# Performance work log

Hardware: AMD Instinct MI355X
Metric: run time of the kernel (lower is better)

Reference implementation:

```python
import jax, jax.numpy as jnp
import numpy as np

POOL = 7  # adaptive_avg_pool2d output size (7,7)


def _bin_edges(start, length):
    """Adaptive-avg-pool bin boundaries.
    start, length: [N] int32 -> (lo, hi) each [N, POOL] absolute indices,
    matching torch: lo_i = floor(i*L/P), hi_i = ceil((i+1)*L/P).
    """
    i = jnp.arange(POOL, dtype=jnp.int32)
    lo = start[:, None] + (i[None, :] * length[:, None]) // POOL
    hi = start[:, None] + (-((-(i[None, :] + 1)) * length[:, None] // POOL))
    # note: ceil(a/b) = -(-a // b); written below explicitly
    hi = start[:, None] - ((-(i[None, :] + 1) * length[:, None]) // POOL)
    return lo, hi


def roi_adaptive_avg_pool(features, rois):
    """features: [1, C, H, W]; rois: [N, 4] int (x1,y1,x2,y2 inclusive).
    Returns [N, C, POOL, POOL] == torch stack of adaptive_avg_pool2d over
    features[:, :, y1:y2+1, x1:x2+1], vectorized via an integral image.
    """
    B, C, H, W = features.shape  # B == 1 (forced by shared_fcs input dim)
    # integral image with a zero row/col prepended: ii[y, x] = sum over [:y, :x]
    ii = jnp.cumsum(jnp.cumsum(features, axis=2), axis=3)
    ii = jnp.pad(ii, ((0, 0), (0, 0), (1, 0), (1, 0)))[0]  # [C, H+1, W+1]

    x1, y1, x2, y2 = rois[:, 0], rois[:, 1], rois[:, 2], rois[:, 3]
    ys, ye = _bin_edges(y1, y2 - y1 + 1)   # [N, POOL]
    xs, xe = _bin_edges(x1, x2 - x1 + 1)
    Y0, Y1 = ys[:, :, None], ye[:, :, None]   # [N, POOL, 1]
    X0, X1 = xs[:, None, :], xe[:, None, :]   # [N, 1, POOL]

    def gather(Y, X):
        return ii[:, Y, X]  # [C, N, POOL, POOL]

    sums = gather(Y1, X1) - gather(Y0, X1) - gather(Y1, X0) + gather(Y0, X0)
    area = ((Y1 - Y0) * (X1 - X0)).astype(features.dtype)  # [N, POOL, POOL]
    pooled = sums / area[None]                              # [C, N, POOL, POOL]
    return jnp.transpose(pooled, (1, 0, 2, 3))              # [N, C, POOL, POOL]


def setup_inputs() -> dict:
    key = jax.random.key(0)
    ks = jax.random.split(key, 12)
    C, H, W, N, F = 256, 336, 336, 2000, 256
    features = jax.random.normal(ks[0], (1, C, H, W), dtype=jnp.float32)
    # valid small ROIs (shuttlecock-sized), x1<=x2, y1<=y2, in-bounds
    x1 = jax.random.randint(ks[1], (N,), 0, W - 40)
    y1 = jax.random.randint(ks[2], (N,), 0, H - 40)
    bw = jax.random.randint(ks[3], (N,), 4, 40)
    bh = jax.random.randint(ks[4], (N,), 4, 40)
    rois = jnp.stack([x1, y1, jnp.minimum(x1 + bw, W - 1),
                      jnp.minimum(y1 + bh, H - 1)], axis=1).astype(jnp.int32)
    d_in = C * POOL * POOL
    w1 = jax.random.normal(ks[5], (d_in, F), dtype=jnp.float32) * (1.0 / np.sqrt(d_in))
    b1 = jnp.zeros((F,), dtype=jnp.float32)
    w2 = jax.random.normal(ks[6], (F, F), dtype=jnp.float32) * (1.0 / np.sqrt(F))
    b2 = jnp.zeros((F,), dtype=jnp.float32)
    w_cls = jax.random.normal(ks[7], (F, 2), dtype=jnp.float32) * 0.01
    b_cls = jnp.zeros((2,), dtype=jnp.float32)
    w_reg = jax.random.normal(ks[8], (F, 4), dtype=jnp.float32) * 0.001
    b_reg = jnp.zeros((4,), dtype=jnp.float32)
    return {"features": features, "rois": rois, "w1": w1, "b1": b1,
            "w2": w2, "b2": b2, "w_cls": w_cls, "b_cls": b_cls,
            "w_reg": w_reg, "b_reg": b_reg}


def reference(features, rois, w1, b1, w2, b2, w_cls, b_cls, w_reg, b_reg):
    roi_feats = roi_adaptive_avg_pool(features, rois)          # [N, C, 7, 7]
    roi_feats = roi_feats.reshape(roi_feats.shape[0], -1)      # [N, C*49]
    h = jax.nn.relu(roi_feats @ w1 + b1)
    h = jax.nn.relu(h @ w2 + b2)
    cls_score = h @ w_cls + b_cls                              # [N, num_classes+1]
    bbox_pred = h @ w_reg + b_reg                              # [N, 4]
    return (cls_score, bbox_pred)
```

## Files before the change

kernel.cpp:

```cpp
#include <hip/hip_runtime.h>

typedef unsigned int uint;
typedef unsigned short ushort;
typedef __bf16 v8bf __attribute__((ext_vector_type(8)));
typedef float v4f __attribute__((ext_vector_type(4)));
typedef float f2 __attribute__((ext_vector_type(2)));
typedef float f4v __attribute__((ext_vector_type(4)));

#define CCH 256
#define HH 336
#define WW 336
#define HWSZ (HH*WW)
#define NROI 2000
#define KDIM 12544
#define MPAD 2048
#define SPLITK 7
#define KSP (KDIM/SPLITK)
#define NTRB (HWSZ/64)

__device__ __forceinline__ ushort bf16r(float f) {
  uint u = __float_as_uint(f);
  u += 0x7fffu + ((u >> 16) & 1u);
  return (ushort)(u >> 16);
}
__device__ __forceinline__ uint packbf(float a, float b) {
  return (uint)bf16r(a) | ((uint)bf16r(b) << 16);
}

typedef const __attribute__((address_space(1))) uint* gas_t;
typedef __attribute__((address_space(3))) uint* las_t;
__device__ __forceinline__ void async16(const void* g, void* l) {
  __builtin_amdgcn_global_load_lds((gas_t)g, (las_t)l, 16, 0, 0);
}

#define GLOAD4(dst, ptr)                                             \
  asm volatile("global_load_dwordx4 %0, %1, off" : "=v"(dst) : "v"(ptr))

__global__ __launch_bounds__(256) void k_trprep(const float* __restrict__ f,
                                                uint* __restrict__ ftu,
                                                const float* __restrict__ w1,
                                                uint* __restrict__ w1t_u,
                                                const float* __restrict__ w2,
                                                ushort* __restrict__ w2t,
                                                const int* __restrict__ rois,
                                                int* __restrict__ perm) {
  __shared__ uint SM[64 * 128];
  int tid = threadIdx.x;
  if (blockIdx.x < NTRB) {
    uint* T = SM;
    int hw0 = blockIdx.x * 64;
    int hwq = tid & 15;
    int cp = tid >> 4;
    const float* base = f + hw0 + hwq * 4;
    f4v va[8], vb[8];
#pragma unroll
    for (int j = 0; j < 8; ++j) {
      int cpair = j * 16 + cp;
      const float* pa = base + (size_t)(2 * cpair) * HWSZ;
      GLOAD4(va[j], pa);
      GLOAD4(vb[j], pa + HWSZ);
    }
    asm volatile("s_waitcnt vmcnt(0)" ::: "memory");
    __builtin_amdgcn_sched_barrier(0);
    int sw = (hwq & 7) << 2;
#pragma unroll
    for (int j = 0; j < 8; ++j) {
      int cs = (j * 16 + cp) ^ sw;
      T[(hwq * 4 + 0) * 128 + cs] = packbf(va[j].x, vb[j].x);
      T[(hwq * 4 + 1) * 128 + cs] = packbf(va[j].y, vb[j].y);
      T[(hwq * 4 + 2) * 128 + cs] = packbf(va[j].z, vb[j].z);
      T[(hwq * 4 + 3) * 128 + cs] = packbf(va[j].w, vb[j].w);
    }
    __syncthreads();
    int co = tid & 31, r = tid >> 5;
#pragma unroll
    for (int i = 0; i < 8; ++i) {
      int row = i * 8 + r;
      int col = (co * 4) ^ (((row >> 2) & 7) << 2);
      uint4 v = *(const uint4*)&T[row * 128 + col];
      *(uint4*)(ftu + (size_t)(hw0 + row) * 128 + co * 4) = v;
    }
    return;
  }
  int b = blockIdx.x - NTRB;
  if (b < 392) {
    ushort (*T)[258] = reinterpret_cast<ushort (*)[258]>(SM);
    int bin = b % 49;
    int c0 = (b / 49) * 32;
    int n = tid;
    for (int i = 0; i < 32; ++i)
      T[i][n] = bf16r(w1[(size_t)((c0 + i) * 49 + bin) * 256 + n]);
    __syncthreads();
    int cc = tid & 15;
    int nb = tid >> 4;
    for (int rep = 0; rep < 16; ++rep) {
      int nn = rep * 16 + nb;
      uint v = (uint)T[2 * cc][nn] | ((uint)T[2 * cc + 1][nn] << 16);
      w1t_u[(size_t)nn * (KDIM / 2) + bin * 128 + c0 / 2 + cc] = v;
    }
  } else if (b < 424) {
    int n = (b - 392) * 8 + (tid >> 5);
    for (int kl = 0; kl < 8; ++kl) {
      int k = kl * 32 + (tid & 31);
      w2t[n * 256 + k] = bf16r(w2[k * 256 + n]);
    }
  } else {
    int* hist = (int*)((char*)SM + 16512);
    int* keys = hist + 64;
    if (tid < 64) hist[tid] = 0;
    __syncthreads();
    for (int i = tid; i < NROI; i += 256) {
      int x1 = rois[i * 4 + 0], y1 = rois[i * 4 + 1];
      int x2 = rois[i * 4 + 2], y2 = rois[i * 4 + 3];
      int cx = (x1 + x2) >> 1, cy = (y1 + y2) >> 1;
      int k = (cy / 42) * 8 + (cx / 42);
      keys[i] = k;
      atomicAdd(&hist[k], 1);
    }
    __syncthreads();
    if (tid < 64) {
      int v = hist[tid];
      int s = v;
#pragma unroll
      for (int d = 1; d < 64; d <<= 1) {
        int t2 = __shfl_up(s, d, 64);
        if (tid >= d) s += t2;
      }
      hist[tid] = s - v;
    }
    __syncthreads();
    for (int i = tid; i < NROI; i += 256) {
      int pos = atomicAdd(&hist[keys[i]], 1);
      perm[pos] = i;
    }
  }
}

__device__ __forceinline__ void pkacc(f2& acc, uint u) {
  f2 t;
  t.x = __uint_as_float(u << 16);
  t.y = __uint_as_float(u & 0xffff0000u);
  asm("v_pk_add_f32 %0, %1, %0" : "+v"(acc) : "v"(t));
}
#define UNPK2(S, u) do { pkacc(S[0], (u).x); pkacc(S[1], (u).y); } while (0)

#define GLOAD2(dst, ptr, OFF)                                        \
  asm volatile("global_load_dwordx2 %0, %1, off offset:" #OFF        \
               : "=v"(dst) : "v"(ptr))

template <int RH>
__device__ __forceinline__ void pool_unit(const uint2* __restrict__ ftu2,
                                          uint2* __restrict__ rfu2,
                                          int x1, int Lw, int ylo, int lane,
                                          uint ob) {
  const uint2* pr[RH];
#pragma unroll
  for (int r = 0; r < RH; ++r)
    pr[r] = ftu2 + (size_t)((ylo + r) * WW + x1) * 64 + lane;
  int xend = x1 + Lw;
  int b = 0;
  int lo_cur = x1;
  int hi_cur = x1 + (Lw + 6) / 7;
  int lo_next = x1 + Lw / 7;
  f2 P[2], Lc[2], Ln[2];
  P[0] = (f2){0.f, 0.f}; P[1] = (f2){0.f, 0.f};
  Lc[0] = (f2){0.f, 0.f}; Lc[1] = (f2){0.f, 0.f};
  Ln[0] = (f2){0.f, 0.f}; Ln[1] = (f2){0.f, 0.f};
  const float invr = 1.0f / (float)RH;
  for (int xc = x1; xc < xend; xc += 4) {
    uint2 v[4][RH];
#pragma unroll
    for (int r = 0; r < RH; ++r) {
      GLOAD2(v[0][r], pr[r], 0);
      GLOAD2(v[1][r], pr[r], 512);
      GLOAD2(v[2][r], pr[r], 1024);
      GLOAD2(v[3][r], pr[r], 1536);
    }
    asm volatile("s_waitcnt vmcnt(0)" ::: "memory");
    __builtin_amdgcn_sched_barrier(0);
#pragma unroll
    for (int r = 0; r < RH; ++r) pr[r] += 256;
#pragma unroll
    for (int c = 0; c < 4; ++c) {
      int x = xc + c;
      if (x < xend) {
#pragma unroll
        for (int r = 0; r < RH; ++r) UNPK2(P, v[c][r]);
        int xp = x + 1;
        if (xp == lo_next) { Ln[0] = P[0]; Ln[1] = P[1]; }
        while (b < 7 && xp == hi_cur) {
          float inv = invr / (float)(hi_cur - lo_cur);
          uint2 o;
          o.x = packbf((P[0].x - Lc[0].x) * inv, (P[0].y - Lc[0].y) * inv);
          o.y = packbf((P[1].x - Lc[1].x) * inv, (P[1].y - Lc[1].y) * inv);
          rfu2[ob + b * 64] = o;
          ++b;
          Lc[0] = Ln[0]; Lc[1] = Ln[1];
          lo_cur = lo_next;
          hi_cur = x1 + ((b + 1) * Lw + 6) / 7;
          lo_next = x1 + ((b + 1) * Lw) / 7;
          if (xp == lo_next) { Ln[0] = P[0]; Ln[1] = P[1]; }
        }
      }
    }
  }
}

__global__ __launch_bounds__(64) void k_pool(const int* __restrict__ rois,
                                             const int* __restrict__ perm,
                                             const uint2* __restrict__ ftu2,
                                             uint2* __restrict__ rfu2) {
  int L = blockIdx.x;
  int i = L >> 3;
  int slot = (L & 7) * 250 + i / 7;
  int by = i % 7;
  int n = perm[slot];
  int lane = threadIdx.x;
  int x1 = rois[n * 4 + 0], y1 = rois[n * 4 + 1];
  int x2 = rois[n * 4 + 2], y2 = rois[n * 4 + 3];
  int Lw = x2 - x1 + 1, Lh = y2 - y1 + 1;
  int ylo = y1 + (by * Lh) / 7;
  int yhi = y1 + ((by + 1) * Lh + 6) / 7;
  int rh = yhi - ylo;
  uint ob = ((uint)n * 49 + (uint)by * 7) * 64 + lane;
  switch (rh) {
    case 1: pool_unit<1>(ftu2, rfu2, x1, Lw, ylo, lane, ob); break;
    case 2: pool_unit<2>(ftu2, rfu2, x1, Lw, ylo, lane, ob); break;
    case 3: pool_unit<3>(ftu2, rfu2, x1, Lw, ylo, lane, ob); break;
    case 4: pool_unit<4>(ftu2, rfu2, x1, Lw, ylo, lane, ob); break;
    case 5: pool_unit<5>(ftu2, rfu2, x1, Lw, ylo, lane, ob); break;
    case 6: pool_unit<6>(ftu2, rfu2, x1, Lw, ylo, lane, ob); break;
    default: pool_unit<7>(ftu2, rfu2, x1, Lw, ylo, lane, ob); break;
  }
}

__global__ __launch_bounds__(256) void k_gemm1(const ushort* __restrict__ A,
                                               const ushort* __restrict__ B,
                                               float* __restrict__ P) {
  __shared__ ushort As[64 * 64];
  __shared__ ushort Bs[128 * 64];
  int m0 = blockIdx.x * 64;
  int n0 = blockIdx.y * 128;
  int ks = blockIdx.z;
  int k0 = ks * KSP;
  int tid = threadIdx.x;
  int lane = tid & 63, wv = tid >> 6;
  int wm = wv & 1, wn = wv >> 1;
  int lm = lane & 15, quad = lane >> 4;
  int srow = tid >> 3, scol = (tid & 7) * 8;
  v4f acc[2][4];
#pragma unroll
  for (int i = 0; i < 2; ++i)
#pragma unroll
    for (int j = 0; j < 4; ++j) acc[i][j] = (v4f){0.f, 0.f, 0.f, 0.f};
  const ushort* Ab = A + (size_t)(m0 + srow) * KDIM + k0 + scol;
  const ushort* Bb = B + (size_t)(n0 + srow) * KDIM + k0 + scol;
  for (int kt = 0; kt < KSP / 64; ++kt) {
    __syncthreads();
#pragma unroll
    for (int r = 0; r < 2; ++r)
      async16(Ab + (size_t)(r * 32) * KDIM + kt * 64, &As[(srow + r * 32) * 64 + scol]);
#pragma unroll
    for (int r = 0; r < 4; ++r)
      async16(Bb + (size_t)(r * 32) * KDIM + kt * 64, &Bs[(srow + r * 32) * 64 + scol]);
    __syncthreads();
#pragma unroll
    for (int kk = 0; kk < 64; kk += 32) {
      v8bf a[2], b[4];
#pragma unroll
      for (int i = 0; i < 2; ++i)
        a[i] = *(const v8bf*)&As[(wm * 32 + i * 16 + lm) * 64 + kk + quad * 8];
#pragma unroll
      for (int j = 0; j < 4; ++j)
        b[j] = *(const v8bf*)&Bs[(wn * 64 + j * 16 + lm) * 64 + kk + quad * 8];
#pragma unroll
      for (int i = 0; i < 2; ++i)
#pragma unroll
        for (int j = 0; j < 4; ++j)
          acc[i][j] = __builtin_amdgcn_mfma_f32_16x16x32_bf16(a[i], b[j], acc[i][j], 0, 0, 0);
    }
  }
  float* Pb = P + (size_t)ks * MPAD * 256;
#pragma unroll
  for (int i = 0; i < 2; ++i)
#pragma unroll
    for (int j = 0; j < 4; ++j) {
      int row = m0 + wm * 32 + i * 16 + quad * 4;
      int col = n0 + wn * 64 + j * 16 + lm;
#pragma unroll
      for (int r = 0; r < 4; ++r)
        Pb[(size_t)(row + r) * 256 + col] = acc[i][j][r];
    }
}

__global__ __launch_bounds__(256) void k_gemm2(const float* __restrict__ P,
                                               const float* __restrict__ b1,
                                               const ushort* __restrict__ w2t,
                                               const float* __restrict__ b2,
                                               const float* __restrict__ wcls,
                                               const float* __restrict__ bcls,
                                               const float* __restrict__ wreg,
                                               const float* __restrict__ breg,
                                               float* __restrict__ out) {
  __shared__ ushort HsA[64 * 256];
  __shared__ ushort Bs2[256 * 64];
  __shared__ float Hs[64 * 257];
  int tid = threadIdx.x;
  int r0 = blockIdx.x * 64;
  int lane = tid & 63, wv = tid >> 6;
  int lm = lane & 15, quad = lane >> 4;
  int srow = tid >> 3, scol = (tid & 7) * 8;
  uint* H = (uint*)HsA;
  for (int it = 0; it < 16; ++it) {
    int e = it * 256 + tid;
    int row = e >> 6;
    int c4 = e & 63;
    float4 s = {0.f, 0.f, 0.f, 0.f};
#pragma unroll
    for (int ks = 0; ks < SPLITK; ++ks) {
      float4 v = ((const float4*)P)[((size_t)ks * MPAD + r0 + row) * 64 + c4];
      s.x += v.x; s.y += v.y; s.z += v.z; s.w += v.w;
    }
    int col = c4 * 4;
    s.x = fmaxf(s.x + b1[col + 0], 0.f);
    s.y = fmaxf(s.y + b1[col + 1], 0.f);
    s.z = fmaxf(s.z + b1[col + 2], 0.f);
    s.w = fmaxf(s.w + b1[col + 3], 0.f);
    int cs = (c4 >> 1) ^ (row & 7);
    int ui = row * 128 + cs * 4 + (c4 & 1) * 2;
    H[ui]     = packbf(s.x, s.y);
    H[ui + 1] = packbf(s.z, s.w);
  }
  v4f acc[16];
#pragma unroll
  for (int j = 0; j < 16; ++j) acc[j] = (v4f){0.f, 0.f, 0.f, 0.f};
  int arow = wv * 16 + lm;
  int asw = (arow & 7) << 3;
  for (int kt = 0; kt < 4; ++kt) {
    __syncthreads();
#pragma unroll
    for (int r = 0; r < 8; ++r)
      async16(w2t + (size_t)(srow + r * 32) * 256 + kt * 64 + scol,
              &Bs2[(srow + r * 32) * 64 + scol]);
    __syncthreads();
#pragma unroll
    for (int kk = 0; kk < 64; kk += 32) {
      v8bf a = *(const v8bf*)&HsA[arow * 256 + ((kt * 64 + kk + quad * 8) ^ asw)];
#pragma unroll
      for (int j = 0; j < 16; ++j) {
        v8bf b = *(const v8bf*)&Bs2[(j * 16 + lm) * 64 + kk + quad * 8];
        acc[j] = __builtin_amdgcn_mfma_f32_16x16x32_bf16(a, b, acc[j], 0, 0, 0);
      }
    }
  }
#pragma unroll
  for (int j = 0; j < 16; ++j) {
    int nn = j * 16 + lm;
    float bb = b2[nn];
#pragma unroll
    for (int r = 0; r < 4; ++r) {
      int row = wv * 16 + quad * 4 + r;
      Hs[row * 257 + nn] = fmaxf(acc[j][r] + bb, 0.f);
    }
  }
  __syncthreads();
  for (int o = tid; o < 384; o += 256) {
    int hd = o >> 6, r = o & 63;
    int grow = r0 + r;
    float d = 0.f;
    if (hd < 2) {
      for (int k = 0; k < 256; ++k) d += Hs[r * 257 + k] * wcls[k * 2 + hd];
      d += bcls[hd];
      if (grow < NROI) out[grow * 2 + hd] = d;
    } else {
      int h4 = hd - 2;
      for (int k = 0; k < 256; ++k) d += Hs[r * 257 + k] * wreg[k * 4 + h4];
      d += breg[h4];
      if (grow < NROI) out[4000 + grow * 4 + h4] = d;
    }
  }
}

extern "C" void kernel_launch(void* const* d_in, const int* in_sizes, int n_in,
                              void* d_out, int out_size, void* d_ws, size_t ws_size,
                              hipStream_t stream) {
  const float* features = (const float*)d_in[0];
  const int* rois = (const int*)d_in[1];
  const float* w1 = (const float*)d_in[2];
  const float* b1 = (const float*)d_in[3];
  const float* w2 = (const float*)d_in[4];
  const float* b2 = (const float*)d_in[5];
  const float* wcls = (const float*)d_in[6];
  const float* bcls = (const float*)d_in[7];
  const float* wreg = (const float*)d_in[8];
  const float* breg = (const float*)d_in[9];
  char* ws = (char*)d_ws;
  ushort* ft  = (ushort*)(ws + 0);
  ushort* w1t = (ushort*)(ws + 57802752);
  ushort* w2t = (ushort*)(ws + 64225280);
  ushort* rf  = (ushort*)(ws + 64356352);
  int*    perm = (int*)(ws + 64356352 + (size_t)NROI * KDIM * 2);
  float*  P   = (float*)(ws + 115736576);
  float* out = (float*)d_out;

  hipLaunchKernelGGL(k_trprep, dim3(NTRB + 425), dim3(256), 0, stream,
                     features, (uint*)ft, w1, (uint*)w1t, w2, w2t, rois, perm);
  hipLaunchKernelGGL(k_pool, dim3(NROI * 7), dim3(64), 0, stream, rois, perm,
                     (const uint2*)ft, (uint2*)rf);
  hipLaunchKernelGGL(k_gemm1, dim3(32, 2, SPLITK), dim3(256), 0, stream, rf, w1t, P);
  hipLaunchKernelGGL(k_gemm2, dim3(32), dim3(256), 0, stream, P, b1, w2t, b2,
                     wcls, bcls, wreg, breg, out);
}
```

Measured before the change: 331.0 us.

## Double-buffer feature loads in ROI pooling for short bin heights

Adds a double-buffered variant of the per-row-band pooling loop that issues the next chunk of global loads before consuming the current one, waiting with partial vmcnt counts. For small bin heights (1-2 rows) the chunk width grows to 8 columns. Taller bins keep a single-buffered path so register pressure stays bounded. The aim is to hide memory latency in the latency-bound pooling kernel, at the cost of more registers and possibly lower occupancy.

New measurement: 332.8 us (median of 2 runs). No clear change (+0.6%).

```diff
diff --git a/kernel.cpp b/kernel.cpp
--- a/kernel.cpp
+++ b/kernel.cpp
@@ -144,65 +144,134 @@
 }
 #define UNPK2(S, u) do { pkacc(S[0], (u).x); pkacc(S[1], (u).y); } while (0)
 
-#define GLOAD2(dst, ptr, OFF)                                        \
+#define GL(dst, ptr, OFF)                                            \
   asm volatile("global_load_dwordx2 %0, %1, off offset:" #OFF        \
                : "=v"(dst) : "v"(ptr))
 
+template <int N> __device__ __forceinline__ void waitvm() {
+  if constexpr (N == 0)       asm volatile("s_waitcnt vmcnt(0)" ::: "memory");
+  else if constexpr (N == 8)  asm volatile("s_waitcnt vmcnt(8)" ::: "memory");
+  else if constexpr (N == 12) asm volatile("s_waitcnt vmcnt(12)" ::: "memory");
+  else if constexpr (N == 16) asm volatile("s_waitcnt vmcnt(16)" ::: "memory");
+  else                        asm volatile("s_waitcnt vmcnt(0)" ::: "memory");
+}
+
+struct BinState {
+  int b, lo_cur, hi_cur, lo_next;
+  f2 P[2], Lc[2], Ln[2];
+};
+
+template <int RH, int CW>
+__device__ __forceinline__ void issue_chunk(uint2 (&buf)[CW][RH],
+                                            const uint2* (&pr)[RH]) {
+#pragma unroll
+  for (int r = 0; r < RH; ++r) {
+    GL(buf[0][r], pr[r], 0);
+    if constexpr (CW > 1) GL(buf[1][r], pr[r], 512);
+    if constexpr (CW > 2) GL(buf[2][r], pr[r], 1024);
+    if constexpr (CW > 3) GL(buf[3][r], pr[r], 1536);
+    if constexpr (CW > 4) GL(buf[4][r], pr[r], 2048);
+    if constexpr (CW > 5) GL(buf[5][r], pr[r], 2560);
+    if constexpr (CW > 6) GL(buf[6][r], pr[r], 3072);
+    if constexpr (CW > 7) GL(buf[7][r], pr[r], 3584);
+  }
+#pragma unroll
+  for (int r = 0; r < RH; ++r) pr[r] += CW * 64;
+}
+
+template <int RH, int CW>
+__device__ __forceinline__ void consume_chunk(const uint2 (&v)[CW][RH], int xc,
+                                              int xend, int x1, int Lw,
+                                              float invr, uint ob,
+                                              uint2* __restrict__ rfu2,
+                                              BinState& S) {
+#pragma unroll
+  for (int c = 0; c < CW; ++c) {
+    int x = xc + c;
+    if (x < xend) {
+#pragma unroll
+      for (int r = 0; r < RH; ++r) UNPK2(S.P, v[c][r]);
+      int xp = x + 1;
+      if (xp == S.lo_next) { S.Ln[0] = S.P[0]; S.Ln[1] = S.P[1]; }
+      while (S.b < 7 && xp == S.hi_cur) {
+        float inv = invr / (float)(S.hi_cur - S.lo_cur);
+        uint2 o;
+        o.x = packbf((S.P[0].x - S.Lc[0].x) * inv, (S.P[0].y - S.Lc[0].y) * inv);
+        o.y = packbf((S.P[1].x - S.Lc[1].x) * inv, (S.P[1].y - S.Lc[1].y) * inv);
+        rfu2[ob + S.b * 64] = o;
+        ++S.b;
+        S.Lc[0] = S.Ln[0]; S.Lc[1] = S.Ln[1];
+        S.lo_cur = S.lo_next;
+        S.hi_cur = x1 + ((S.b + 1) * Lw + 6) / 7;
+        S.lo_next = x1 + ((S.b + 1) * Lw) / 7;
+        if (xp == S.lo_next) { S.Ln[0] = S.P[0]; S.Ln[1] = S.P[1]; }
+      }
+    }
+  }
+}
+
 template <int RH>
-__device__ __forceinline__ void pool_unit(const uint2* __restrict__ ftu2,
-                                          uint2* __restrict__ rfu2,
-                                          int x1, int Lw, int ylo, int lane,
-                                          uint ob) {
+__device__ __forceinline__ void init_state(BinState& S, int x1, int Lw) {
+  S.b = 0;
+  S.lo_cur = x1;
+  S.hi_cur = x1 + (Lw + 6) / 7;
+  S.lo_next = x1 + Lw / 7;
+  S.P[0] = (f2){0.f, 0.f}; S.P[1] = (f2){0.f, 0.f};
+  S.Lc[0] = (f2){0.f, 0.f}; S.Lc[1] = (f2){0.f, 0.f};
+  S.Ln[0] = (f2){0.f, 0.f}; S.Ln[1] = (f2){0.f, 0.f};
+}
+
+template <int RH, int CW>
+__device__ void pool_db(const uint2* __restrict__ ftu2,
+                        uint2* __restrict__ rfu2,
+                        int x1, int Lw, int ylo, int lane, uint ob) {
   const uint2* pr[RH];
 #pragma unroll
   for (int r = 0; r < RH; ++r)
     pr[r] = ftu2 + (size_t)((ylo + r) * WW + x1) * 64 + lane;
   int xend = x1 + Lw;
-  int b = 0;
-  int lo_cur = x1;
-  int hi_cur = x1 + (Lw + 6) / 7;
-  int lo_next = x1 + Lw / 7;
-  f2 P[2], Lc[2], Ln[2];
-  P[0] = (f2){0.f, 0.f}; P[1] = (f2){0.f, 0.f};
-  Lc[0] = (f2){0.f, 0.f}; Lc[1] = (f2){0.f, 0.f};
-  Ln[0] = (f2){0.f, 0.f}; Ln[1] = (f2){0.f, 0.f};
+  BinState S;
+  init_state<RH>(S, x1, Lw);
   const float invr = 1.0f / (float)RH;
-  for (int xc = x1; xc < xend; xc += 4) {
-    uint2 v[4][RH];
-#pragma unroll
-    for (int r = 0; r < RH; ++r) {
-      GLOAD2(v[0][r], pr[r], 0);
-      GLOAD2(v[1][r], pr[r], 512);
-      GLOAD2(v[2][r], pr[r], 1024);
-      GLOAD2(v[3][r], pr[r], 1536);
-    }
-    asm volatile("s_waitcnt vmcnt(0)" ::: "memory");
+  uint2 va[CW][RH], vb[CW][RH];
+  issue_chunk<RH, CW>(va, pr);
+  int xc = x1;
+  for (;;) {
+    int xn = xc + CW;
+    if (xn < xend) { issue_chunk<RH, CW>(vb, pr); waitvm<CW * RH>(); }
+    else waitvm<0>();
     __builtin_amdgcn_sched_barrier(0);
-#pragma unroll
-    for (int r = 0; r < RH; ++r) pr[r] += 256;
-#pragma unroll
-    for (int c = 0; c < 4; ++c) {
-      int x = xc + c;
-      if (x < xend) {
-#pragma unroll
-        for (int r = 0; r < RH; ++r) UNPK2(P, v[c][r]);
-        int xp = x + 1;
-        if (xp == lo_next) { Ln[0] = P[0]; Ln[1] = P[1]; }
-        while (b < 7 && xp == hi_cur) {
-          float inv = invr / (float)(hi_cur - lo_cur);
-          uint2 o;
-          o.x = packbf((P[0].x - Lc[0].x) * inv, (P[0].y - Lc[0].y) * inv);
-          o.y = packbf((P[1].x - Lc[1].x) * inv, (P[1].y - Lc[1].y) * inv);
-          rfu2[ob + b * 64] = o;
-          ++b;
-          Lc[0] = Ln[0]; Lc[1] = Ln[1];
-          lo_cur = lo_next;
-          hi_cur = x1 + ((b + 1) * Lw + 6) / 7;
-          lo_next = x1 + ((b + 1) * Lw) / 7;
-          if (xp == lo_next) { Ln[0] = P[0]; Ln[1] = P[1]; }
-        }
-      }
-    }
+    consume_chunk<RH, CW>(va, xc, xend, x1, Lw, invr, ob, rfu2, S);
+    if (xn >= xend) return;
+    xc = xn;
+    xn = xc + CW;
+    if (xn < xend) { issue_chunk<RH, CW>(va, pr); waitvm<CW * RH>(); }
+    else waitvm<0>();
+    __builtin_amdgcn_sched_barrier(0);
+    consume_chunk<RH, CW>(vb, xc, xend, x1, Lw, invr, ob, rfu2, S);
+    if (xn >= xend) return;
+    xc = xn;
+  }
+}
+
+template <int RH, int CW>
+__device__ void pool_sb(const uint2* __restrict__ ftu2,
+                        uint2* __restrict__ rfu2,
+                        int x1, int Lw, int ylo, int lane, uint ob) {
+  const uint2* pr[RH];
+#pragma unroll
+  for (int r = 0; r < RH; ++r)
+    pr[r] = ftu2 + (size_t)((ylo + r) * WW + x1) * 64 + lane;
+  int xend = x1 + Lw;
+  BinState S;
+  init_state<RH>(S, x1, Lw);
+  const float invr = 1.0f / (float)RH;
+  uint2 va[CW][RH];
+  for (int xc = x1; xc < xend; xc += CW) {
+    issue_chunk<RH, CW>(va, pr);
+    waitvm<0>();
+    __builtin_amdgcn_sched_barrier(0);
+    consume_chunk<RH, CW>(va, xc, xend, x1, Lw, invr, ob, rfu2, S);
   }
 }
 
@@ -224,13 +293,13 @@
   int rh = yhi - ylo;
   uint ob = ((uint)n * 49 + (uint)by * 7) * 64 + lane;
   switch (rh) {
-    case 1: pool_unit<1>(ftu2, rfu2, x1, Lw, ylo, lane, ob); break;
-    case 2: pool_unit<2>(ftu2, rfu2, x1, Lw, ylo, lane, ob); break;
-    case 3: pool_unit<3>(ftu2, rfu2, x1, Lw, ylo, lane, ob); break;
-    case 4: pool_unit<4>(ftu2, rfu2, x1, Lw, ylo, lane, ob); break;
-    case 5: pool_unit<5>(ftu2, rfu2, x1, Lw, ylo, lane, ob); break;
-    case 6: pool_unit<6>(ftu2, rfu2, x1, Lw, ylo, lane, ob); break;
-    default: pool_unit<7>(ftu2, rfu2, x1, Lw, ylo, lane, ob); break;
+    case 1: pool_db<1, 8>(ftu2, rfu2, x1, Lw, ylo, lane, ob); break;
+    case 2: pool_db<2, 8>(ftu2, rfu2, x1, Lw, ylo, lane, ob); break;
+    case 3: pool_db<3, 4>(ftu2, rfu2, x1, Lw, ylo, lane, ob); break;
+    case 4: pool_db<4, 4>(ftu2, rfu2, x1, Lw, ylo, lane, ob); break;
+    case 5: pool_sb<5, 4>(ftu2, rfu2, x1, Lw, ylo, lane, ob); break;
+    case 6: pool_sb<6, 4>(ftu2, rfu2, x1, Lw, ylo, lane, ob); break;
+    default: pool_sb<7, 4>(ftu2, rfu2, x1, Lw, ylo, lane, ob); break;
   }
 }
 
```
